# Optimization experiments

Measured on AMD Instinct MI355X. Metric: run time of the kernel, lower is better.

Reference implementation:

```python
import jax, jax.numpy as jnp
import numpy as np

BN_EPS = 1e-3
BN_SCALE = 1.0 / np.sqrt(1.0 + BN_EPS)  # inference BN with default moving stats (mean=0, var=1)


def _gru(x_seq, h0, Wx, Wh, b):
    """Keras GRU (reset_after=True). x_seq: [B,T,in], h0: [B,u].
    Wx: [in,3u], Wh: [u,3u], b: [2,3u] (input bias, recurrent bias).
    Returns (outputs [B,T,u], h_T [B,u])."""
    # precompute input contributions for all timesteps in one big matmul
    xg = jnp.einsum('bti,ig->btg', x_seq, Wx) + b[0]  # [B,T,3u]
    xg = jnp.moveaxis(xg, 1, 0)  # [T,B,3u] for scan

    def step(h, xt):
        rg = h @ Wh + b[1]  # [B,3u]
        xz, xr, xh = jnp.split(xt, 3, axis=-1)
        rz, rr, rh = jnp.split(rg, 3, axis=-1)
        z = jax.nn.sigmoid(xz + rz)
        r = jax.nn.sigmoid(xr + rr)
        hh = jnp.tanh(xh + r * rh)
        hn = z * h + (1.0 - z) * hh
        return hn, hn

    hT, ys = jax.lax.scan(step, h0, xg)
    return jnp.moveaxis(ys, 0, 1), hT  # [B,T,u], [B,u]


def _encoder(x_ids, h0, E, params):
    xcur = E[x_ids]  # [B,T,d]
    new_hidden = []
    out = xcur
    for i, (Wxf, Whf, bf, Wxb, Whb, bb) in enumerate(params):
        fw_out, fw_h = _gru(xcur, h0[i, 0], Wxf, Whf, bf)
        bw_out, bw_h = _gru(xcur[:, ::-1, :], h0[i, 1], Wxb, Whb, bb)
        # BN(training=False) with fresh layers == scale by 1/sqrt(1+eps)
        out = jnp.concatenate([fw_out * BN_SCALE, bw_out * BN_SCALE], axis=2)
        new_hidden.append(jnp.stack([fw_h, bw_h], axis=0))
        xcur = out
    # final BN on each direction hidden state
    new_hidden = jnp.stack(new_hidden, axis=0) * BN_SCALE  # [L,2,B,u]
    return out, new_hidden


def setup_inputs() -> dict:
    key = jax.random.key(0)
    ks = jax.random.split(key, 16)
    B, T, V, D, U = 32, 256, 32000, 512, 512
    s = 0.1
    inp = {
        'x': jax.random.randint(ks[0], (B, T), 0, V, dtype=jnp.int64)
             if jax.config.jax_enable_x64 else jax.random.randint(ks[0], (B, T), 0, V, dtype=jnp.int32),
        'h0': jnp.zeros((2, 2, B, U), jnp.float32),
        'E': jax.random.normal(ks[1], (V, D), jnp.float32) * s,
        'Wx0f': jax.random.normal(ks[2], (D, 3 * U), jnp.float32) * s,
        'Wh0f': jax.random.normal(ks[3], (U, 3 * U), jnp.float32) * s,
        'b0f': jax.random.normal(ks[4], (2, 3 * U), jnp.float32) * s,
        'Wx0b': jax.random.normal(ks[5], (D, 3 * U), jnp.float32) * s,
        'Wh0b': jax.random.normal(ks[6], (U, 3 * U), jnp.float32) * s,
        'b0b': jax.random.normal(ks[7], (2, 3 * U), jnp.float32) * s,
        'Wx1f': jax.random.normal(ks[8], (2 * U, 3 * U), jnp.float32) * s,
        'Wh1f': jax.random.normal(ks[9], (U, 3 * U), jnp.float32) * s,
        'b1f': jax.random.normal(ks[10], (2, 3 * U), jnp.float32) * s,
        'Wx1b': jax.random.normal(ks[11], (2 * U, 3 * U), jnp.float32) * s,
        'Wh1b': jax.random.normal(ks[12], (U, 3 * U), jnp.float32) * s,
        'b1b': jax.random.normal(ks[13], (2, 3 * U), jnp.float32) * s,
    }
    return inp


def reference(x, h0, E, Wx0f, Wh0f, b0f, Wx0b, Wh0b, b0b,
              Wx1f, Wh1f, b1f, Wx1b, Wh1b, b1b):
    params = [(Wx0f, Wh0f, b0f, Wx0b, Wh0b, b0b),
              (Wx1f, Wh1f, b1f, Wx1b, Wh1b, b1b)]
    return _encoder(x, h0, E, params)
```

## Files before the change

kernel.cpp:

```cpp
#include <hip/hip_runtime.h>
#include <hip/hip_bf16.h>


typedef __attribute__((ext_vector_type(8))) short short8;
typedef __attribute__((ext_vector_type(8))) __bf16 bf16x8;
typedef __attribute__((ext_vector_type(4))) float f32x4;
typedef __attribute__((ext_vector_type(4))) int i32x4;
typedef __attribute__((ext_vector_type(2))) float f32x2;

#define DEVINLINE __device__ __forceinline__

static constexpr int B = 32, T = 256, U = 512, NG = 1536;
static constexpr int BU = B * U;
static constexpr long OUT_ELEMS = 8388608;
static constexpr float SCALE_BN = 0.9995003746879552f;

DEVINLINE unsigned bfbits(float f) {
  unsigned u = __float_as_uint(f);
  return (u + 0x7fffu + ((u >> 16) & 1u)) >> 16;
}
DEVINLINE float bf2f(unsigned bits) { return __uint_as_float(bits << 16); }
DEVINLINE void split2(float v, unsigned& hi, unsigned& lo) {
  hi = bfbits(v);
  lo = bfbits(v - bf2f(hi));
}
DEVINLINE float sigmoidf_(float x) { return 1.f / (1.f + __expf(-x)); }
DEVINLINE float tanhf_(float x) {
  x = fminf(15.f, fmaxf(-15.f, x));
  float e = __expf(2.f * x);
  return (e - 1.f) / (e + 1.f);
}
DEVINLINE f32x4 mfma16(short8 a, short8 b, f32x4 c) {
  return __builtin_amdgcn_mfma_f32_16x16x32_bf16(
      __builtin_bit_cast(bf16x8, a), __builtin_bit_cast(bf16x8, b), c, 0, 0, 0);
}

__global__ __launch_bounds__(256)
void transpose_w(const float* __restrict__ in, unsigned short* __restrict__ oh,
                 unsigned short* __restrict__ ol, int K, int N) {
  __shared__ float tile[32][33];
  const int n0 = blockIdx.x * 32, k0 = blockIdx.y * 32;
  const int tx = threadIdx.x & 31, ty = threadIdx.x >> 5;
  for (int i = ty; i < 32; i += 8)
    tile[i][tx] = in[(long)(k0 + i) * N + n0 + tx];
  __syncthreads();
  for (int i = ty; i < 32; i += 8) {
    const float v = tile[tx][i];
    unsigned hi, lo;
    split2(v, hi, lo);
    oh[(long)(n0 + i) * K + k0 + tx] = (unsigned short)hi;
    ol[(long)(n0 + i) * K + k0 + tx] = (unsigned short)lo;
  }
}

__global__ __launch_bounds__(256)
void embed_kernel(const int* __restrict__ x, const float* __restrict__ E,
                  unsigned short* __restrict__ xh, unsigned short* __restrict__ xl) {
  const int r = blockIdx.x;
  const int t = r >> 5, b = r & 31;
  const int id = x[b * T + t];
  const float* src = E + (long)id * 512;
  f32x2 v = *reinterpret_cast<const f32x2*>(src + threadIdx.x * 2);
  unsigned h0, l0, h1, l1;
  split2(v.x, h0, l0);
  split2(v.y, h1, l1);
  ((unsigned*)xh)[(long)r * 256 + threadIdx.x] = h0 | (h1 << 16);
  ((unsigned*)xl)[(long)r * 256 + threadIdx.x] = l0 | (l1 << 16);
}

template <int K>
__global__ __launch_bounds__(256)
void gemm_bias(const unsigned short* __restrict__ Ah,
               const unsigned short* __restrict__ Al,
               const unsigned short* __restrict__ Bh,
               const unsigned short* __restrict__ Bl,
               const float* __restrict__ bias, float* __restrict__ C) {
  __shared__ __align__(16) unsigned short AsH[128 * 32];
  __shared__ __align__(16) unsigned short BsH[128 * 32];
  __shared__ __align__(16) unsigned short AsL[128 * 32];
  __shared__ __align__(16) unsigned short BsL[128 * 32];
  const int m0 = blockIdx.x * 128, n0 = blockIdx.y * 128;
  const int tid = threadIdx.x, lane = tid & 63, wave = tid >> 6;
  const int wr = wave >> 1, wc = wave & 1, lr = lane & 15, kq = lane >> 4;
  f32x4 acc[4][4] = {};
  for (int kt = 0; kt < K / 32; ++kt) {
    const int k0 = kt * 32;
    i32x4 vah[2], vbh[2], val[2], vbl[2];
#pragma unroll
    for (int u = 0; u < 2; ++u) {
      const int idx = tid + u * 256, row = idx >> 2, sub = idx & 3;
      vah[u] = *reinterpret_cast<const i32x4*>(Ah + (long)(m0 + row) * K + k0 + sub * 8);
      vbh[u] = *reinterpret_cast<const i32x4*>(Bh + (long)(n0 + row) * K + k0 + sub * 8);
      val[u] = *reinterpret_cast<const i32x4*>(Al + (long)(m0 + row) * K + k0 + sub * 8);
      vbl[u] = *reinterpret_cast<const i32x4*>(Bl + (long)(n0 + row) * K + k0 + sub * 8);
    }
    __syncthreads();
#pragma unroll
    for (int u = 0; u < 2; ++u) {
      const int idx = tid + u * 256;
      *reinterpret_cast<i32x4*>(AsH + idx * 8) = vah[u];
      *reinterpret_cast<i32x4*>(BsH + idx * 8) = vbh[u];
      *reinterpret_cast<i32x4*>(AsL + idx * 8) = val[u];
      *reinterpret_cast<i32x4*>(BsL + idx * 8) = vbl[u];
    }
    __syncthreads();
    short8 afh[4], bfh[4], afl[4], bfl[4];
#pragma unroll
    for (int i = 0; i < 4; ++i) {
      afh[i] = *reinterpret_cast<const short8*>(AsH + (wr * 64 + i * 16 + lr) * 32 + kq * 8);
      bfh[i] = *reinterpret_cast<const short8*>(BsH + (wc * 64 + i * 16 + lr) * 32 + kq * 8);
      afl[i] = *reinterpret_cast<const short8*>(AsL + (wr * 64 + i * 16 + lr) * 32 + kq * 8);
      bfl[i] = *reinterpret_cast<const short8*>(BsL + (wc * 64 + i * 16 + lr) * 32 + kq * 8);
    }
#pragma unroll
    for (int i = 0; i < 4; ++i)
#pragma unroll
      for (int j = 0; j < 4; ++j) {
        acc[i][j] = mfma16(afh[i], bfh[j], acc[i][j]);
        acc[i][j] = mfma16(afh[i], bfl[j], acc[i][j]);
        acc[i][j] = mfma16(afl[i], bfh[j], acc[i][j]);
      }
  }
#pragma unroll
  for (int j = 0; j < 4; ++j) {
    const int col = n0 + wc * 64 + j * 16 + lr;
    const float bv = bias[col];
#pragma unroll
    for (int i = 0; i < 4; ++i) {
      const int row0 = m0 + wr * 64 + i * 16 + kq * 4;
#pragma unroll
      for (int r = 0; r < 4; ++r)
        C[(long)(row0 + r) * NG + col] = acc[i][j][r] + bv;
    }
  }
}

__global__ __launch_bounds__(384, 1)
void gru_scan(const float* __restrict__ xgf, const float* __restrict__ xgb,
              const unsigned short* __restrict__ whtfh,
              const unsigned short* __restrict__ whtfl,
              const unsigned short* __restrict__ whtbh,
              const unsigned short* __restrict__ whtbl,
              const float* __restrict__ rbf, const float* __restrict__ rbb,
              const float* __restrict__ h0L,
              unsigned short* __restrict__ hbh,
              unsigned short* __restrict__ hbl,
              int* __restrict__ flags,
              unsigned short* __restrict__ out0h,
              unsigned short* __restrict__ out0l,
              float* __restrict__ outF,
              float* __restrict__ hT,
              const int layer) {
  const int dir = blockIdx.x >> 4, wg = blockIdx.x & 15;
  const int j0 = wg * 32;
  const int tid = threadIdx.x, wave = tid >> 6, lane = tid & 63;
  const int lr = lane & 15, kq = lane >> 4;
  const float* xg = dir ? xgb : xgf;
  const unsigned short* wth = dir ? whtbh : whtfh;
  const unsigned short* wtl = dir ? whtbl : whtfl;
  const float* rb = dir ? rbb : rbf;
  const float* h0d = h0L + dir * BU;
  unsigned short* hbhd = hbh + dir * 2 * BU;
  unsigned short* hbld = hbl + dir * 2 * BU;
  int* flg = flags + dir * 16;

  __shared__ __align__(16) unsigned short h_hi[32][544];
  __shared__ __align__(16) unsigned short h_lo[32][544];
  __shared__ float rg_lds[32][97];

  const int g = wave >> 1, half = wave & 1;
  const int c0 = g * 512 + j0 + half * 16;
  short8 wfh[16], wfl[16];
#pragma unroll
  for (int kk = 0; kk < 16; ++kk) {
    wfh[kk] = *reinterpret_cast<const short8*>(wth + (long)(c0 + lr) * 512 + kk * 32 + kq * 8);
    wfl[kk] = *reinterpret_cast<const short8*>(wtl + (long)(c0 + lr) * 512 + kk * 32 + kq * 8);
  }
  const float bv = rb[c0 + lr];

  float hpr[2][2];
#pragma unroll
  for (int q = 0; q < 2; ++q) {
    const int p = tid + q * 384;
    if (p < 512) {
      const int b = p >> 4, jr = (p & 15) * 2;
      hpr[q][0] = h0d[b * U + j0 + jr];
      hpr[q][1] = h0d[b * U + j0 + jr + 1];
    }
  }

  f32x2 xv[2][3];
  auto load_xv = [&](int t_in) {
    const long xbase = (long)t_in * 32 * NG;
#pragma unroll
    for (int q = 0; q < 2; ++q) {
      const int p = tid + q * 384;
      if (p < 512) {
        const int b = p >> 4, jr = (p & 15) * 2;
#pragma unroll
        for (int gg = 0; gg < 3; ++gg)
          xv[q][gg] = *reinterpret_cast<const f32x2*>(
              xg + xbase + (long)b * NG + gg * 512 + j0 + jr);
      }
    }
  };
  load_xv(dir ? (T - 1) : 0);

  for (int s = 0; s < T; ++s) {
    const int par = s & 1;

    if (s == 0) {
      for (int p = tid; p < BU / 4; p += 384) {
        const int b = p >> 7, u = (p & 127) * 4;
        f32x4 v = *reinterpret_cast<const f32x4*>(h0d + b * U + u);
        unsigned hi0, lo0, hi1, lo1, hi2, lo2, hi3, lo3;
        split2(v.x, hi0, lo0); split2(v.y, hi1, lo1);
        split2(v.z, hi2, lo2); split2(v.w, hi3, lo3);
        unsigned* dh = reinterpret_cast<unsigned*>(&h_hi[b][u]);
        unsigned* dl = reinterpret_cast<unsigned*>(&h_lo[b][u]);
        dh[0] = hi0 | (hi1 << 16); dh[1] = hi2 | (hi3 << 16);
        dl[0] = lo0 | (lo1 << 16); dl[1] = lo2 | (lo3 << 16);
      }
    } else {
      const unsigned long long* hsh =
          (const unsigned long long*)(hbhd + par * BU);
      const unsigned long long* hsl =
          (const unsigned long long*)(hbld + par * BU);
      for (int p = tid; p < BU / 4; p += 384) {
        const int b = p >> 7, u = (p & 127) * 4;
        unsigned long long vh = __hip_atomic_load(
            hsh + (b * U + u) / 4, __ATOMIC_RELAXED, __HIP_MEMORY_SCOPE_AGENT);
        unsigned long long vl = __hip_atomic_load(
            hsl + (b * U + u) / 4, __ATOMIC_RELAXED, __HIP_MEMORY_SCOPE_AGENT);
        *reinterpret_cast<unsigned long long*>(&h_hi[b][u]) = vh;
        *reinterpret_cast<unsigned long long*>(&h_lo[b][u]) = vl;
      }
    }
    __syncthreads();

    f32x4 aHH0 = {}, aHL0 = {}, aLH0 = {}, aHH1 = {}, aHL1 = {}, aLH1 = {};
#pragma unroll
    for (int kk = 0; kk < 16; ++kk) {
      const short8 a0h = *reinterpret_cast<const short8*>(&h_hi[lr][kk * 32 + kq * 8]);
      const short8 a0l = *reinterpret_cast<const short8*>(&h_lo[lr][kk * 32 + kq * 8]);
      const short8 a1h = *reinterpret_cast<const short8*>(&h_hi[16 + lr][kk * 32 + kq * 8]);
      const short8 a1l = *reinterpret_cast<const short8*>(&h_lo[16 + lr][kk * 32 + kq * 8]);
      aHH0 = mfma16(a0h, wfh[kk], aHH0);
      aHL0 = mfma16(a0h, wfl[kk], aHL0);
      aLH0 = mfma16(a0l, wfh[kk], aLH0);
      aHH1 = mfma16(a1h, wfh[kk], aHH1);
      aHL1 = mfma16(a1h, wfl[kk], aHL1);
      aLH1 = mfma16(a1l, wfh[kk], aLH1);
    }
#pragma unroll
    for (int r = 0; r < 4; ++r) {
      rg_lds[kq * 4 + r][wave * 16 + lr] = aHH0[r] + aHL0[r] + aLH0[r] + bv;
      rg_lds[16 + kq * 4 + r][wave * 16 + lr] = aHH1[r] + aHL1[r] + aLH1[r] + bv;
    }
    __syncthreads();

    unsigned* hdh = (unsigned*)(hbhd + (1 - par) * BU);
    unsigned* hdl = (unsigned*)(hbld + (1 - par) * BU);
#pragma unroll
    for (int q = 0; q < 2; ++q) {
      const int p = tid + q * 384;
      if (p >= 512) break;
      const int b = p >> 4, jr = (p & 15) * 2;
      float hn[2];
#pragma unroll
      for (int e = 0; e < 2; ++e) {
        const int j = jr + e;
        const float xz = xv[q][0][e], xr = xv[q][1][e], xh = xv[q][2][e];
        const float rz = rg_lds[b][j], rr = rg_lds[b][32 + j], rh = rg_lds[b][64 + j];
        const float z = sigmoidf_(xz + rz);
        const float r = sigmoidf_(xr + rr);
        const float hh = tanhf_(xh + r * rh);
        hn[e] = z * hpr[q][e] + (1.f - z) * hh;
      }
      hpr[q][0] = hn[0];
      hpr[q][1] = hn[1];
      unsigned hi0, lo0, hi1, lo1;
      split2(hn[0], hi0, lo0); split2(hn[1], hi1, lo1);
      __hip_atomic_store(hdh + (b * U + j0 + jr) / 2, hi0 | (hi1 << 16),
                         __ATOMIC_RELAXED, __HIP_MEMORY_SCOPE_AGENT);
      __hip_atomic_store(hdl + (b * U + j0 + jr) / 2, lo0 | (lo1 << 16),
                         __ATOMIC_RELAXED, __HIP_MEMORY_SCOPE_AGENT);
      if (layer == 0) {
        const float o0 = hn[0] * SCALE_BN, o1 = hn[1] * SCALE_BN;
        unsigned oh0, ol0, oh1, ol1;
        split2(o0, oh0, ol0); split2(o1, oh1, ol1);
        const long oidx = (((long)s * 32 + b) * 1024 + dir * 512 + j0 + jr) >> 1;
        ((unsigned*)out0h)[oidx] = oh0 | (oh1 << 16);
        ((unsigned*)out0l)[oidx] = ol0 | (ol1 << 16);
      } else {
        float* o = outF + ((long)b * T + s) * 1024 + dir * 512 + j0 + jr;
        o[0] = hn[0] * SCALE_BN;
        o[1] = hn[1] * SCALE_BN;
      }
      if (s == T - 1) {
        float* o = hT + dir * BU + b * U + j0 + jr;
        o[0] = hn[0] * SCALE_BN;
        o[1] = hn[1] * SCALE_BN;
      }
    }
    asm volatile("s_waitcnt vmcnt(0)" ::: "memory");
    __syncthreads();
    if (tid == 0)
      __hip_atomic_store(flg + wg, s + 1, __ATOMIC_RELAXED, __HIP_MEMORY_SCOPE_AGENT);
    if (s < T - 1) {
      load_xv(dir ? (T - 2 - s) : (s + 1));
      if (tid < 16) {
        while (__hip_atomic_load(flg + tid, __ATOMIC_RELAXED, __HIP_MEMORY_SCOPE_AGENT) < s + 1)
          __builtin_amdgcn_s_sleep(1);
      }
      __syncthreads();
    }
  }
}

extern "C" void kernel_launch(void* const* d_in, const int* in_sizes, int n_in,
                              void* d_out, int out_size, void* d_ws, size_t ws_size,
                              hipStream_t stream) {
  (void)in_sizes; (void)n_in; (void)out_size; (void)ws_size;
  const int*   x    = (const int*)d_in[0];
  const float* h0   = (const float*)d_in[1];
  const float* E    = (const float*)d_in[2];
  const float* Wx0f = (const float*)d_in[3];
  const float* Wh0f = (const float*)d_in[4];
  const float* b0f  = (const float*)d_in[5];
  const float* Wx0b = (const float*)d_in[6];
  const float* Wh0b = (const float*)d_in[7];
  const float* b0b  = (const float*)d_in[8];
  const float* Wx1f = (const float*)d_in[9];
  const float* Wh1f = (const float*)d_in[10];
  const float* b1f  = (const float*)d_in[11];
  const float* Wx1b = (const float*)d_in[12];
  const float* Wh1b = (const float*)d_in[13];
  const float* b1b  = (const float*)d_in[14];
  float* dout = (float*)d_out;

  char* p = (char*)d_ws;
  auto alloc = [&p](long bytes) { char* r = p; p += (bytes + 255) & ~255L; return r; };
  float* XGF = (float*)alloc(50331648);
  float* XGB = (float*)alloc(50331648);
  unsigned short* OUT0H = (unsigned short*)alloc(16777216);
  unsigned short* OUT0L = (unsigned short*)alloc(16777216);
  unsigned short* X0H = OUT0H;
  unsigned short* X0L = OUT0L;
  unsigned short* WHT0FH = (unsigned short*)alloc(1572864);
  unsigned short* WHT0FL = (unsigned short*)alloc(1572864);
  unsigned short* WHT0BH = (unsigned short*)alloc(1572864);
  unsigned short* WHT0BL = (unsigned short*)alloc(1572864);
  unsigned short* WHT1FH = (unsigned short*)alloc(1572864);
  unsigned short* WHT1FL = (unsigned short*)alloc(1572864);
  unsigned short* WHT1BH = (unsigned short*)alloc(1572864);
  unsigned short* WHT1BL = (unsigned short*)alloc(1572864);
  unsigned short* WXT0FH = (unsigned short*)alloc(1572864);
  unsigned short* WXT0FL = (unsigned short*)alloc(1572864);
  unsigned short* WXT0BH = (unsigned short*)alloc(1572864);
  unsigned short* WXT0BL = (unsigned short*)alloc(1572864);
  unsigned short* WXT1FH = (unsigned short*)alloc(3145728);
  unsigned short* WXT1FL = (unsigned short*)alloc(3145728);
  unsigned short* WXT1BH = (unsigned short*)alloc(3145728);
  unsigned short* WXT1BL = (unsigned short*)alloc(3145728);
  unsigned short* HBH = (unsigned short*)alloc(131072);
  unsigned short* HBL = (unsigned short*)alloc(131072);
  int* FLAGS = (int*)alloc(256);

  hipMemsetAsync(FLAGS, 0, 256, stream);

  dim3 blk(256);
  transpose_w<<<dim3(48, 16), blk, 0, stream>>>(Wh0f, WHT0FH, WHT0FL, 512, NG);
  transpose_w<<<dim3(48, 16), blk, 0, stream>>>(Wh0b, WHT0BH, WHT0BL, 512, NG);
  transpose_w<<<dim3(48, 16), blk, 0, stream>>>(Wh1f, WHT1FH, WHT1FL, 512, NG);
  transpose_w<<<dim3(48, 16), blk, 0, stream>>>(Wh1b, WHT1BH, WHT1BL, 512, NG);
  transpose_w<<<dim3(48, 16), blk, 0, stream>>>(Wx0f, WXT0FH, WXT0FL, 512, NG);
  transpose_w<<<dim3(48, 16), blk, 0, stream>>>(Wx0b, WXT0BH, WXT0BL, 512, NG);
  transpose_w<<<dim3(48, 32), blk, 0, stream>>>(Wx1f, WXT1FH, WXT1FL, 1024, NG);
  transpose_w<<<dim3(48, 32), blk, 0, stream>>>(Wx1b, WXT1BH, WXT1BL, 1024, NG);

  embed_kernel<<<dim3(8192), blk, 0, stream>>>(x, E, X0H, X0L);

  gemm_bias<512><<<dim3(64, 12), blk, 0, stream>>>(
      X0H, X0L, WXT0FH, WXT0FL, b0f, XGF);
  gemm_bias<512><<<dim3(64, 12), blk, 0, stream>>>(
      X0H, X0L, WXT0BH, WXT0BL, b0b, XGB);
  gru_scan<<<dim3(32), dim3(384), 0, stream>>>(
      XGF, XGB, WHT0FH, WHT0FL, WHT0BH, WHT0BL, b0f + NG, b0b + NG, h0,
      HBH, HBL, FLAGS, OUT0H, OUT0L, nullptr, dout + OUT_ELEMS, 0);

  gemm_bias<1024><<<dim3(64, 12), blk, 0, stream>>>(
      OUT0H, OUT0L, WXT1FH, WXT1FL, b1f, XGF);
  gemm_bias<1024><<<dim3(64, 12), blk, 0, stream>>>(
      OUT0H, OUT0L, WXT1BH, WXT1BL, b1b, XGB);
  gru_scan<<<dim3(32), dim3(384), 0, stream>>>(
      XGF, XGB, WHT1FH, WHT1FL, WHT1BH, WHT1BL, b1f + NG, b1b + NG, h0 + 2 * BU,
      HBH, HBL, FLAGS + 32, nullptr, nullptr, dout, dout + OUT_ELEMS + 2 * BU, 1);
}
```

Measured before the change: 3.972 ms.

## Warp-specialize GRU scan with loader waves and per-chunk LDS readiness flags

The block grows to 12 waves, and 4 of them become dedicated loaders. Each loader polls the per-workgroup flags for its 32-column chunk and copies that chunk of the hidden state into a double-buffered LDS array. It then signals readiness per chunk, so the MFMA waves can start on chunks that are already available instead of waiting for the whole state. Block-wide __syncthreads is replaced by an 8-wave atomic counter barrier, and the three accumulators per row tile are merged into one. This targets the serialization of the global barrier, the full-state reload and the matmul in each time step. The cost is spin-waits on LDS atomics and subtle ordering correctness between loader and compute waves.

```diff
diff --git a/kernel.cpp b/kernel.cpp
--- a/kernel.cpp
+++ b/kernel.cpp
@@ -14,6 +14,7 @@
 static constexpr int BU = B * U;
 static constexpr long OUT_ELEMS = 8388608;
 static constexpr float SCALE_BN = 0.9995003746879552f;
+static constexpr int HSTR = 520;
 
 DEVINLINE unsigned bfbits(float f) {
   unsigned u = __float_as_uint(f);
@@ -135,7 +136,14 @@
   }
 }
 
-__global__ __launch_bounds__(384, 1)
+DEVINLINE void sync8(int* cnt, int target) {
+  if ((threadIdx.x & 63) == 0)
+    __hip_atomic_fetch_add(cnt, 1, __ATOMIC_RELEASE, __HIP_MEMORY_SCOPE_WORKGROUP);
+  while (__hip_atomic_load(cnt, __ATOMIC_ACQUIRE, __HIP_MEMORY_SCOPE_WORKGROUP) < target) {
+  }
+}
+
+__global__ __launch_bounds__(768, 1)
 void gru_scan(const float* __restrict__ xgf, const float* __restrict__ xgb,
               const unsigned short* __restrict__ whtfh,
               const unsigned short* __restrict__ whtfl,
@@ -164,157 +172,164 @@
   unsigned short* hbld = hbl + dir * 2 * BU;
   int* flg = flags + dir * 16;
 
-  __shared__ __align__(16) unsigned short h_hi[32][544];
-  __shared__ __align__(16) unsigned short h_lo[32][544];
+  __shared__ __align__(16) unsigned short h_lds[2][2][32][HSTR];
   __shared__ float rg_lds[32][97];
-
-  const int g = wave >> 1, half = wave & 1;
-  const int c0 = g * 512 + j0 + half * 16;
+  __shared__ int ld_ready[16];
+  __shared__ int s8cnt[2];
+
+  if (tid < 16) ld_ready[tid] = 0;
+  if (tid < 2) s8cnt[tid] = 0;
+  __syncthreads();
+
+  if (wave >= 8) {
+    const int lw = wave - 8;
+    for (int s = 0; s < T; ++s) {
+      const int par = s & 1;
+      const unsigned short* hsh = hbhd + par * BU;
+      const unsigned short* hsl = hbld + par * BU;
+#pragma unroll
+      for (int idx = 0; idx < 4; ++idx) {
+        const int j = lw + idx * 4;
+        if (s == 0) {
+#pragma unroll
+          for (int i = 0; i < 4; ++i) {
+            const int c = i * 64 + lane, b = c >> 3, ch = (c & 7) * 4;
+            f32x4 v = *reinterpret_cast<const f32x4*>(h0d + b * U + j * 32 + ch);
+            unsigned h0b, l0b, h1b, l1b, h2b, l2b, h3b, l3b;
+            split2(v.x, h0b, l0b); split2(v.y, h1b, l1b);
+            split2(v.z, h2b, l2b); split2(v.w, h3b, l3b);
+            union { unsigned long long u; unsigned w[2]; } ph, pl;
+            ph.w[0] = h0b | (h1b << 16); ph.w[1] = h2b | (h3b << 16);
+            pl.w[0] = l0b | (l1b << 16); pl.w[1] = l2b | (l3b << 16);
+            *reinterpret_cast<unsigned long long*>(&h_lds[0][0][b][j * 32 + ch]) = ph.u;
+            *reinterpret_cast<unsigned long long*>(&h_lds[0][1][b][j * 32 + ch]) = pl.u;
+          }
+        } else {
+          while (__hip_atomic_load(flg + j, __ATOMIC_RELAXED,
+                                   __HIP_MEMORY_SCOPE_AGENT) < s)
+            __builtin_amdgcn_s_sleep(1);
+#pragma unroll
+          for (int i = 0; i < 4; ++i) {
+            const int c = i * 64 + lane, b = c >> 3, ch = (c & 7) * 4;
+            unsigned long long vh = __hip_atomic_load(
+                (const unsigned long long*)(hsh + b * U + j * 32 + ch),
+                __ATOMIC_RELAXED, __HIP_MEMORY_SCOPE_AGENT);
+            unsigned long long vl = __hip_atomic_load(
+                (const unsigned long long*)(hsl + b * U + j * 32 + ch),
+                __ATOMIC_RELAXED, __HIP_MEMORY_SCOPE_AGENT);
+            *reinterpret_cast<unsigned long long*>(&h_lds[par][0][b][j * 32 + ch]) = vh;
+            *reinterpret_cast<unsigned long long*>(&h_lds[par][1][b][j * 32 + ch]) = vl;
+          }
+        }
+        __hip_atomic_store(&ld_ready[j], s + 1, __ATOMIC_RELEASE,
+                           __HIP_MEMORY_SCOPE_WORKGROUP);
+      }
+    }
+    return;
+  }
+
   short8 wfh[16], wfl[16];
-#pragma unroll
-  for (int kk = 0; kk < 16; ++kk) {
-    wfh[kk] = *reinterpret_cast<const short8*>(wth + (long)(c0 + lr) * 512 + kk * 32 + kq * 8);
-    wfl[kk] = *reinterpret_cast<const short8*>(wtl + (long)(c0 + lr) * 512 + kk * 32 + kq * 8);
-  }
-  const float bv = rb[c0 + lr];
-
-  float hpr[2][2];
-#pragma unroll
-  for (int q = 0; q < 2; ++q) {
-    const int p = tid + q * 384;
-    if (p < 512) {
-      const int b = p >> 4, jr = (p & 15) * 2;
-      hpr[q][0] = h0d[b * U + j0 + jr];
-      hpr[q][1] = h0d[b * U + j0 + jr + 1];
-    }
-  }
-
-  f32x2 xv[2][3];
+  float bv = 0.f;
+  if (wave < 6) {
+    const int g = wave >> 1, half = wave & 1;
+    const int c0 = g * 512 + j0 + half * 16;
+#pragma unroll
+    for (int kk = 0; kk < 16; ++kk) {
+      wfh[kk] = *reinterpret_cast<const short8*>(wth + (long)(c0 + lr) * 512 + kk * 32 + kq * 8);
+      wfl[kk] = *reinterpret_cast<const short8*>(wtl + (long)(c0 + lr) * 512 + kk * 32 + kq * 8);
+    }
+    bv = rb[c0 + lr];
+  }
+
+  const int gb = tid >> 4, gjr = (tid & 15) * 2;
+  float hpr[2];
+  hpr[0] = h0d[gb * U + j0 + gjr];
+  hpr[1] = h0d[gb * U + j0 + gjr + 1];
+
+  f32x2 xv[3];
   auto load_xv = [&](int t_in) {
     const long xbase = (long)t_in * 32 * NG;
 #pragma unroll
-    for (int q = 0; q < 2; ++q) {
-      const int p = tid + q * 384;
-      if (p < 512) {
-        const int b = p >> 4, jr = (p & 15) * 2;
-#pragma unroll
-        for (int gg = 0; gg < 3; ++gg)
-          xv[q][gg] = *reinterpret_cast<const f32x2*>(
-              xg + xbase + (long)b * NG + gg * 512 + j0 + jr);
-      }
-    }
+    for (int gg = 0; gg < 3; ++gg)
+      xv[gg] = *reinterpret_cast<const f32x2*>(
+          xg + xbase + (long)gb * NG + gg * 512 + j0 + gjr);
   };
   load_xv(dir ? (T - 1) : 0);
 
   for (int s = 0; s < T; ++s) {
     const int par = s & 1;
 
-    if (s == 0) {
-      for (int p = tid; p < BU / 4; p += 384) {
-        const int b = p >> 7, u = (p & 127) * 4;
-        f32x4 v = *reinterpret_cast<const f32x4*>(h0d + b * U + u);
-        unsigned hi0, lo0, hi1, lo1, hi2, lo2, hi3, lo3;
-        split2(v.x, hi0, lo0); split2(v.y, hi1, lo1);
-        split2(v.z, hi2, lo2); split2(v.w, hi3, lo3);
-        unsigned* dh = reinterpret_cast<unsigned*>(&h_hi[b][u]);
-        unsigned* dl = reinterpret_cast<unsigned*>(&h_lo[b][u]);
-        dh[0] = hi0 | (hi1 << 16); dh[1] = hi2 | (hi3 << 16);
-        dl[0] = lo0 | (lo1 << 16); dl[1] = lo2 | (lo3 << 16);
-      }
-    } else {
-      const unsigned long long* hsh =
-          (const unsigned long long*)(hbhd + par * BU);
-      const unsigned long long* hsl =
-          (const unsigned long long*)(hbld + par * BU);
-      for (int p = tid; p < BU / 4; p += 384) {
-        const int b = p >> 7, u = (p & 127) * 4;
-        unsigned long long vh = __hip_atomic_load(
-            hsh + (b * U + u) / 4, __ATOMIC_RELAXED, __HIP_MEMORY_SCOPE_AGENT);
-        unsigned long long vl = __hip_atomic_load(
-            hsl + (b * U + u) / 4, __ATOMIC_RELAXED, __HIP_MEMORY_SCOPE_AGENT);
-        *reinterpret_cast<unsigned long long*>(&h_hi[b][u]) = vh;
-        *reinterpret_cast<unsigned long long*>(&h_lo[b][u]) = vl;
-      }
-    }
-    __syncthreads();
-
-    f32x4 aHH0 = {}, aHL0 = {}, aLH0 = {}, aHH1 = {}, aHL1 = {}, aLH1 = {};
-#pragma unroll
-    for (int kk = 0; kk < 16; ++kk) {
-      const short8 a0h = *reinterpret_cast<const short8*>(&h_hi[lr][kk * 32 + kq * 8]);
-      const short8 a0l = *reinterpret_cast<const short8*>(&h_lo[lr][kk * 32 + kq * 8]);
-      const short8 a1h = *reinterpret_cast<const short8*>(&h_hi[16 + lr][kk * 32 + kq * 8]);
-      const short8 a1l = *reinterpret_cast<const short8*>(&h_lo[16 + lr][kk * 32 + kq * 8]);
-      aHH0 = mfma16(a0h, wfh[kk], aHH0);
-      aHL0 = mfma16(a0h, wfl[kk], aHL0);
-      aLH0 = mfma16(a0l, wfh[kk], aLH0);
-      aHH1 = mfma16(a1h, wfh[kk], aHH1);
-      aHL1 = mfma16(a1h, wfl[kk], aHL1);
-      aLH1 = mfma16(a1l, wfh[kk], aLH1);
-    }
-#pragma unroll
-    for (int r = 0; r < 4; ++r) {
-      rg_lds[kq * 4 + r][wave * 16 + lr] = aHH0[r] + aHL0[r] + aLH0[r] + bv;
-      rg_lds[16 + kq * 4 + r][wave * 16 + lr] = aHH1[r] + aHL1[r] + aLH1[r] + bv;
-    }
-    __syncthreads();
-
-    unsigned* hdh = (unsigned*)(hbhd + (1 - par) * BU);
-    unsigned* hdl = (unsigned*)(hbld + (1 - par) * BU);
-#pragma unroll
-    for (int q = 0; q < 2; ++q) {
-      const int p = tid + q * 384;
-      if (p >= 512) break;
-      const int b = p >> 4, jr = (p & 15) * 2;
+    if (wave < 6) {
+      f32x4 acc0 = {0.f, 0.f, 0.f, 0.f}, acc1 = {0.f, 0.f, 0.f, 0.f};
+#pragma unroll
+      for (int kk = 0; kk < 16; ++kk) {
+        while (__hip_atomic_load(&ld_ready[kk], __ATOMIC_ACQUIRE,
+                                 __HIP_MEMORY_SCOPE_WORKGROUP) < s + 1) {
+        }
+        const short8 a0h = *reinterpret_cast<const short8*>(&h_lds[par][0][lr][kk * 32 + kq * 8]);
+        const short8 a0l = *reinterpret_cast<const short8*>(&h_lds[par][1][lr][kk * 32 + kq * 8]);
+        const short8 a1h = *reinterpret_cast<const short8*>(&h_lds[par][0][16 + lr][kk * 32 + kq * 8]);
+        const short8 a1l = *reinterpret_cast<const short8*>(&h_lds[par][1][16 + lr][kk * 32 + kq * 8]);
+        acc0 = mfma16(a0h, wfh[kk], acc0);
+        acc0 = mfma16(a0h, wfl[kk], acc0);
+        acc0 = mfma16(a0l, wfh[kk], acc0);
+        acc1 = mfma16(a1h, wfh[kk], acc1);
+        acc1 = mfma16(a1h, wfl[kk], acc1);
+        acc1 = mfma16(a1l, wfh[kk], acc1);
+      }
+#pragma unroll
+      for (int r = 0; r < 4; ++r) {
+        rg_lds[kq * 4 + r][wave * 16 + lr] = acc0[r] + bv;
+        rg_lds[16 + kq * 4 + r][wave * 16 + lr] = acc1[r] + bv;
+      }
+    }
+    sync8(&s8cnt[0], 8 * (s + 1));
+
+    {
       float hn[2];
 #pragma unroll
       for (int e = 0; e < 2; ++e) {
-        const int j = jr + e;
-        const float xz = xv[q][0][e], xr = xv[q][1][e], xh = xv[q][2][e];
-        const float rz = rg_lds[b][j], rr = rg_lds[b][32 + j], rh = rg_lds[b][64 + j];
+        const int j = gjr + e;
+        const float xz = xv[0][e], xr = xv[1][e], xh = xv[2][e];
+        const float rz = rg_lds[gb][j], rr = rg_lds[gb][32 + j], rh = rg_lds[gb][64 + j];
         const float z = sigmoidf_(xz + rz);
         const float r = sigmoidf_(xr + rr);
         const float hh = tanhf_(xh + r * rh);
-        hn[e] = z * hpr[q][e] + (1.f - z) * hh;
-      }
-      hpr[q][0] = hn[0];
-      hpr[q][1] = hn[1];
+        hn[e] = z * hpr[e] + (1.f - z) * hh;
+      }
+      hpr[0] = hn[0];
+      hpr[1] = hn[1];
       unsigned hi0, lo0, hi1, lo1;
       split2(hn[0], hi0, lo0); split2(hn[1], hi1, lo1);
-      __hip_atomic_store(hdh + (b * U + j0 + jr) / 2, hi0 | (hi1 << 16),
+      unsigned* hdh = (unsigned*)(hbhd + (1 - par) * BU);
+      unsigned* hdl = (unsigned*)(hbld + (1 - par) * BU);
+      __hip_atomic_store(hdh + (gb * U + j0 + gjr) / 2, hi0 | (hi1 << 16),
                          __ATOMIC_RELAXED, __HIP_MEMORY_SCOPE_AGENT);
-      __hip_atomic_store(hdl + (b * U + j0 + jr) / 2, lo0 | (lo1 << 16),
+      __hip_atomic_store(hdl + (gb * U + j0 + gjr) / 2, lo0 | (lo1 << 16),
                          __ATOMIC_RELAXED, __HIP_MEMORY_SCOPE_AGENT);
       if (layer == 0) {
         const float o0 = hn[0] * SCALE_BN, o1 = hn[1] * SCALE_BN;
         unsigned oh0, ol0, oh1, ol1;
         split2(o0, oh0, ol0); split2(o1, oh1, ol1);
-        const long oidx = (((long)s * 32 + b) * 1024 + dir * 512 + j0 + jr) >> 1;
+        const long oidx = (((long)s * 32 + gb) * 1024 + dir * 512 + j0 + gjr) >> 1;
         ((unsigned*)out0h)[oidx] = oh0 | (oh1 << 16);
         ((unsigned*)out0l)[oidx] = ol0 | (ol1 << 16);
       } else {
-        float* o = outF + ((long)b * T + s) * 1024 + dir * 512 + j0 + jr;
+        float* o = outF + ((long)gb * T + s) * 1024 + dir * 512 + j0 + gjr;
         o[0] = hn[0] * SCALE_BN;
         o[1] = hn[1] * SCALE_BN;
       }
       if (s == T - 1) {
-        float* o = hT + dir * BU + b * U + j0 + jr;
+        float* o = hT + dir * BU + gb * U + j0 + gjr;
         o[0] = hn[0] * SCALE_BN;
         o[1] = hn[1] * SCALE_BN;
       }
     }
     asm volatile("s_waitcnt vmcnt(0)" ::: "memory");
-    __syncthreads();
+    sync8(&s8cnt[1], 8 * (s + 1));
     if (tid == 0)
       __hip_atomic_store(flg + wg, s + 1, __ATOMIC_RELAXED, __HIP_MEMORY_SCOPE_AGENT);
-    if (s < T - 1) {
-      load_xv(dir ? (T - 2 - s) : (s + 1));
-      if (tid < 16) {
-        while (__hip_atomic_load(flg + tid, __ATOMIC_RELAXED, __HIP_MEMORY_SCOPE_AGENT) < s + 1)
-          __builtin_amdgcn_s_sleep(1);
-      }
-      __syncthreads();
-    }
+    if (s < T - 1) load_xv(dir ? (T - 2 - s) : (s + 1));
   }
 }
 
@@ -385,7 +400,7 @@
       X0H, X0L, WXT0FH, WXT0FL, b0f, XGF);
   gemm_bias<512><<<dim3(64, 12), blk, 0, stream>>>(
       X0H, X0L, WXT0BH, WXT0BL, b0b, XGB);
-  gru_scan<<<dim3(32), dim3(384), 0, stream>>>(
+  gru_scan<<<dim3(32), dim3(768), 0, stream>>>(
       XGF, XGB, WHT0FH, WHT0FL, WHT0BH, WHT0BL, b0f + NG, b0b + NG, h0,
       HBH, HBL, FLAGS, OUT0H, OUT0L, nullptr, dout + OUT_ELEMS, 0);
 
@@ -393,7 +408,7 @@
       OUT0H, OUT0L, WXT1FH, WXT1FL, b1f, XGF);
   gemm_bias<1024><<<dim3(64, 12), blk, 0, stream>>>(
       OUT0H, OUT0L, WXT1BH, WXT1BL, b1b, XGB);
-  gru_scan<<<dim3(32), dim3(384), 0, stream>>>(
+  gru_scan<<<dim3(32), dim3(768), 0, stream>>>(
       XGF, XGB, WHT1FH, WHT1FL, WHT1BH, WHT1BL, b1f + NG, b1b + NG, h0 + 2 * BU,
       HBH, HBL, FLAGS + 32, nullptr, nullptr, dout, dout + OUT_ELEMS + 2 * BU, 1);
 }
```

After: 4.852 ms. +22.2%, slower.

## Interleave hidden-state hi/lo planes per block and pad sync flags to cache lines

Applied to the files above, without the earlier changes.

Merges the separate hi/lo hidden-state exchange buffers into one interleaved buffer. Each workgroup's hi and lo bf16 halves for a batch row are now stored contiguously, so the per-step global loads and stores are grouped by producer block. The per-workgroup step flags are spaced 128 bytes apart so spinning readers do not share cache lines with other flags. The LDS row stride shrinks from 544 to 520, which changes bank mapping and LDS footprint; the stride change also risks bank conflicts.

```diff
diff --git a/kernel.cpp b/kernel.cpp
--- a/kernel.cpp
+++ b/kernel.cpp
@@ -14,6 +14,7 @@
 static constexpr int BU = B * U;
 static constexpr long OUT_ELEMS = 8388608;
 static constexpr float SCALE_BN = 0.9995003746879552f;
+static constexpr int HSTR = 520;
 
 DEVINLINE unsigned bfbits(float f) {
   unsigned u = __float_as_uint(f);
@@ -143,8 +144,7 @@
               const unsigned short* __restrict__ whtbl,
               const float* __restrict__ rbf, const float* __restrict__ rbb,
               const float* __restrict__ h0L,
-              unsigned short* __restrict__ hbh,
-              unsigned short* __restrict__ hbl,
+              unsigned long long* __restrict__ hx,
               int* __restrict__ flags,
               unsigned short* __restrict__ out0h,
               unsigned short* __restrict__ out0l,
@@ -160,12 +160,11 @@
   const unsigned short* wtl = dir ? whtbl : whtfl;
   const float* rb = dir ? rbb : rbf;
   const float* h0d = h0L + dir * BU;
-  unsigned short* hbhd = hbh + dir * 2 * BU;
-  unsigned short* hbld = hbl + dir * 2 * BU;
-  int* flg = flags + dir * 16;
-
-  __shared__ __align__(16) unsigned short h_hi[32][544];
-  __shared__ __align__(16) unsigned short h_lo[32][544];
+  unsigned long long* hxd = hx + (long)dir * 2 * 8192;
+  int* flg = flags + dir * 16 * 32;
+
+  __shared__ __align__(16) unsigned short h_hi[32][HSTR];
+  __shared__ __align__(16) unsigned short h_lo[32][HSTR];
   __shared__ float rg_lds[32][97];
 
   const int g = wave >> 1, half = wave & 1;
@@ -222,18 +221,18 @@
         dl[0] = lo0 | (lo1 << 16); dl[1] = lo2 | (lo3 << 16);
       }
     } else {
-      const unsigned long long* hsh =
-          (const unsigned long long*)(hbhd + par * BU);
-      const unsigned long long* hsl =
-          (const unsigned long long*)(hbld + par * BU);
-      for (int p = tid; p < BU / 4; p += 384) {
-        const int b = p >> 7, u = (p & 127) * 4;
-        unsigned long long vh = __hip_atomic_load(
-            hsh + (b * U + u) / 4, __ATOMIC_RELAXED, __HIP_MEMORY_SCOPE_AGENT);
-        unsigned long long vl = __hip_atomic_load(
-            hsl + (b * U + u) / 4, __ATOMIC_RELAXED, __HIP_MEMORY_SCOPE_AGENT);
-        *reinterpret_cast<unsigned long long*>(&h_hi[b][u]) = vh;
-        *reinterpret_cast<unsigned long long*>(&h_lo[b][u]) = vl;
+      const unsigned long long* src = hxd + par * 8192;
+      for (int p = tid; p < 8192; p += 384) {
+        const int blk = p >> 4, sub = p & 15;
+        const int b = blk >> 4, wgs = blk & 15;
+        const int plane = sub >> 3, q8 = sub & 7;
+        unsigned long long v = __hip_atomic_load(
+            src + p, __ATOMIC_RELAXED, __HIP_MEMORY_SCOPE_AGENT);
+        const int u = wgs * 32 + q8 * 4;
+        if (plane == 0)
+          *reinterpret_cast<unsigned long long*>(&h_hi[b][u]) = v;
+        else
+          *reinterpret_cast<unsigned long long*>(&h_lo[b][u]) = v;
       }
     }
     __syncthreads();
@@ -259,8 +258,7 @@
     }
     __syncthreads();
 
-    unsigned* hdh = (unsigned*)(hbhd + (1 - par) * BU);
-    unsigned* hdl = (unsigned*)(hbld + (1 - par) * BU);
+    unsigned* dst = (unsigned*)(hxd + (1 - par) * 8192);
 #pragma unroll
     for (int q = 0; q < 2; ++q) {
       const int p = tid + q * 384;
@@ -281,9 +279,10 @@
       hpr[q][1] = hn[1];
       unsigned hi0, lo0, hi1, lo1;
       split2(hn[0], hi0, lo0); split2(hn[1], hi1, lo1);
-      __hip_atomic_store(hdh + (b * U + j0 + jr) / 2, hi0 | (hi1 << 16),
+      const int blk32 = (b * 16 + wg) * 32 + (jr >> 1);
+      __hip_atomic_store(dst + blk32, hi0 | (hi1 << 16),
                          __ATOMIC_RELAXED, __HIP_MEMORY_SCOPE_AGENT);
-      __hip_atomic_store(hdl + (b * U + j0 + jr) / 2, lo0 | (lo1 << 16),
+      __hip_atomic_store(dst + blk32 + 16, lo0 | (lo1 << 16),
                          __ATOMIC_RELAXED, __HIP_MEMORY_SCOPE_AGENT);
       if (layer == 0) {
         const float o0 = hn[0] * SCALE_BN, o1 = hn[1] * SCALE_BN;
@@ -306,11 +305,13 @@
     asm volatile("s_waitcnt vmcnt(0)" ::: "memory");
     __syncthreads();
     if (tid == 0)
-      __hip_atomic_store(flg + wg, s + 1, __ATOMIC_RELAXED, __HIP_MEMORY_SCOPE_AGENT);
+      __hip_atomic_store(flg + wg * 32, s + 1, __ATOMIC_RELAXED,
+                         __HIP_MEMORY_SCOPE_AGENT);
     if (s < T - 1) {
       load_xv(dir ? (T - 2 - s) : (s + 1));
       if (tid < 16) {
-        while (__hip_atomic_load(flg + tid, __ATOMIC_RELAXED, __HIP_MEMORY_SCOPE_AGENT) < s + 1)
+        while (__hip_atomic_load(flg + tid * 32, __ATOMIC_RELAXED,
+                                 __HIP_MEMORY_SCOPE_AGENT) < s + 1)
           __builtin_amdgcn_s_sleep(1);
       }
       __syncthreads();
@@ -363,11 +364,10 @@
   unsigned short* WXT1FL = (unsigned short*)alloc(3145728);
   unsigned short* WXT1BH = (unsigned short*)alloc(3145728);
   unsigned short* WXT1BL = (unsigned short*)alloc(3145728);
-  unsigned short* HBH = (unsigned short*)alloc(131072);
-  unsigned short* HBL = (unsigned short*)alloc(131072);
-  int* FLAGS = (int*)alloc(256);
-
-  hipMemsetAsync(FLAGS, 0, 256, stream);
+  unsigned long long* HX = (unsigned long long*)alloc(262144);
+  int* FLAGS = (int*)alloc(16384);
+
+  hipMemsetAsync(FLAGS, 0, 16384, stream);
 
   dim3 blk(256);
   transpose_w<<<dim3(48, 16), blk, 0, stream>>>(Wh0f, WHT0FH, WHT0FL, 512, NG);
@@ -387,7 +387,7 @@
       X0H, X0L, WXT0BH, WXT0BL, b0b, XGB);
   gru_scan<<<dim3(32), dim3(384), 0, stream>>>(
       XGF, XGB, WHT0FH, WHT0FL, WHT0BH, WHT0BL, b0f + NG, b0b + NG, h0,
-      HBH, HBL, FLAGS, OUT0H, OUT0L, nullptr, dout + OUT_ELEMS, 0);
+      HX, FLAGS, OUT0H, OUT0L, nullptr, dout + OUT_ELEMS, 0);
 
   gemm_bias<1024><<<dim3(64, 12), blk, 0, stream>>>(
       OUT0H, OUT0L, WXT1FH, WXT1FL, b1f, XGF);
@@ -395,5 +395,5 @@
       OUT0H, OUT0L, WXT1BH, WXT1BL, b1b, XGB);
   gru_scan<<<dim3(32), dim3(384), 0, stream>>>(
       XGF, XGB, WHT1FH, WHT1FL, WHT1BH, WHT1BL, b1f + NG, b1b + NG, h0 + 2 * BU,
-      HBH, HBL, FLAGS + 32, nullptr, nullptr, dout, dout + OUT_ELEMS + 2 * BU, 1);
-}
+      HX, FLAGS + 1024, nullptr, nullptr, dout, dout + OUT_ELEMS + 2 * BU, 1);
+}
```

Result: slower. 5.284 ms (+33.0%).
